# Performance work log

Hardware: AMD Instinct MI355X
Metric: run time of the kernel (lower is better)

## Reference

```python
import jax, jax.numpy as jnp
import numpy as np

WS = 8        # window size
NH = 8        # num heads


def setup_inputs() -> dict:
    key = jax.random.key(0)
    ks = jax.random.split(key, 6)
    B, C, H, W = 8, 256, 64, 64
    Cr = C // 4
    s = lambda n: 1.0 / np.sqrt(n)
    return {
        "x": jax.random.normal(ks[0], (B, C, H, W), jnp.float32),
        "ca_w1": jax.random.normal(ks[1], (Cr, C), jnp.float32) * s(C),
        "ca_b1": jnp.zeros((Cr,), jnp.float32),
        "ca_w2": jax.random.normal(ks[2], (C, Cr), jnp.float32) * s(Cr),
        "ca_b2": jnp.zeros((C,), jnp.float32),
        "in_proj_w": jax.random.normal(ks[3], (3 * C, C), jnp.float32) * s(C),
        "in_proj_b": jnp.zeros((3 * C,), jnp.float32),
        "out_proj_w": jax.random.normal(ks[4], (C, C), jnp.float32) * s(C),
        "out_proj_b": jnp.zeros((C,), jnp.float32),
    }


def reference(x, ca_w1, ca_b1, ca_w2, ca_b2, in_proj_w, in_proj_b, out_proj_w, out_proj_b):
    B, C, H, W = x.shape
    # ---- channel SE gate: AdaptiveAvgPool2d(1) -> 1x1 conv == linear ----
    pooled = x.mean(axis=(2, 3))                                   # [B, C]
    h1 = jax.nn.relu(pooled @ ca_w1.T + ca_b1)                     # [B, C/4]
    ca = jax.nn.sigmoid(h1 @ ca_w2.T + ca_b2)                      # [B, C]
    x = x * ca[:, :, None, None]

    # ---- window partition (non-overlapping unfold) ----
    Hw, Ww = H // WS, W // WS
    nwin = Hw * Ww
    xw = x.reshape(B, C, Hw, WS, Ww, WS).transpose(0, 1, 2, 4, 3, 5)   # [B,C,Hw,Ww,ws,ws]
    # view(B,C,nwin,ws*ws).permute(2,0,3,1).reshape(nwin*B, ws*ws, C)
    xw = xw.reshape(B, C, nwin, WS * WS).transpose(2, 0, 3, 1).reshape(nwin * B, WS * WS, C)

    # ---- nn.MultiheadAttention with batch_first=False: (L, N, E) ----
    # L = nwin*B (sequence!), N = ws*ws (batch!), E = C  -- faithful to source quirk
    L, N, _ = xw.shape
    hd = C // NH
    qkv = xw @ in_proj_w.T + in_proj_b                             # [L, N, 3C]
    q, k, v = jnp.split(qkv, 3, axis=-1)
    to_heads = lambda t: t.reshape(L, N, NH, hd).transpose(1, 2, 0, 3)  # [N, NH, L, hd]
    q, k, v = to_heads(q), to_heads(k), to_heads(v)
    scale = 1.0 / jnp.sqrt(jnp.asarray(hd, x.dtype))
    attn = jax.nn.softmax(jnp.einsum("nhld,nhmd->nhlm", q * scale, k), axis=-1)
    o = jnp.einsum("nhlm,nhmd->nhld", attn, v)                     # [N, NH, L, hd]
    o = o.transpose(2, 0, 1, 3).reshape(L, N, C)
    o = o @ out_proj_w.T + out_proj_b                              # [L, N, C]

    # ---- reshape back; nearest interpolate H*W -> H*W is identity ----
    o = o.reshape(nwin, B, WS * WS, C).transpose(1, 3, 0, 2)       # [B, C, nwin, ws*ws]
    x_out = o.reshape(B, C, H, W)
    return x + x_out
```

## Files before the change

kernel.cpp:

```cpp
#include <hip/hip_runtime.h>
#include <hip/hip_bf16.h>
#include <math.h>


typedef unsigned short ushort_t;
typedef unsigned int uint_t;
typedef __attribute__((ext_vector_type(8))) short bf16x8;
typedef __attribute__((ext_vector_type(4))) float f32x4;

__device__ __forceinline__ uint_t pk_trunc(float a, float b) {
    union { float f; uint_t u; } ua, ub; ua.f = a; ub.f = b;
    return (ua.u >> 16) | (ub.u & 0xffff0000u);
}

__device__ __forceinline__ uint_t pk_rne(float a, float b) {
    __hip_bfloat16 ha = __float2bfloat16(a), hb = __float2bfloat16(b);
    ushort_t ua = *(ushort_t*)&ha, ub = *(ushort_t*)&hb;
    return (uint_t)ua | ((uint_t)ub << 16);
}

__device__ __forceinline__ void gl_lds16(const ushort_t* g, ushort_t* l) {
    __builtin_amdgcn_global_load_lds(
        (__attribute__((address_space(1))) unsigned int*)(g),
        (__attribute__((address_space(3))) unsigned int*)(l), 16, 0, 0);
}

__global__ __launch_bounds__(256) void k_pool(const float* __restrict__ x,
                                              float* __restrict__ pooled) {
    int bc = blockIdx.x;
    const float4* row4 = (const float4*)(x + (size_t)bc * 4096);
    float s = 0.f;
    for (int i = threadIdx.x; i < 1024; i += 256) {
        float4 v = row4[i];
        s += v.x + v.y + v.z + v.w;
    }
    __shared__ float red[256];
    red[threadIdx.x] = s;
    __syncthreads();
    for (int o = 128; o > 0; o >>= 1) {
        if (threadIdx.x < o) red[threadIdx.x] += red[threadIdx.x + o];
        __syncthreads();
    }
    if (threadIdx.x == 0) pooled[bc] = red[0] * (1.f / 4096.f);
}

__global__ __launch_bounds__(256) void k_se(const float* __restrict__ pooled,
                                            const float* __restrict__ w1,
                                            const float* __restrict__ b1,
                                            const float* __restrict__ w2,
                                            const float* __restrict__ b2,
                                            float* __restrict__ ca) {
    __shared__ float sp[2048];
    __shared__ float sh1[512];
    int t = threadIdx.x;
    for (int i = t; i < 2048; i += 256) sp[i] = pooled[i];
    __syncthreads();
    for (int o = t; o < 512; o += 256) {
        int b = o >> 6, m = o & 63;
        float s = b1[m];
        const float* wr = w1 + (size_t)m * 256;
        const float* pr = sp + b * 256;
        for (int c = 0; c < 256; c++) s += pr[c] * wr[c];
        sh1[o] = s > 0.f ? s : 0.f;
    }
    __syncthreads();
    for (int o = t; o < 2048; o += 256) {
        int b = o >> 8, m = o & 255;
        float s = b2[m];
        const float* wr = w2 + (size_t)m * 64;
        const float* hr = sh1 + b * 64;
        for (int c = 0; c < 64; c++) s += hr[c] * wr[c];
        ca[o] = 1.f / (1.f + __expf(-s));
    }
}

__global__ __launch_bounds__(256) void k_cvt(const float* __restrict__ src,
                                             ushort_t* __restrict__ dst, int n8) {
    int i = blockIdx.x * 256 + threadIdx.x;
    if (i >= n8) return;
    const float4* s = (const float4*)src + (size_t)i * 2;
    float4 a = s[0], b = s[1];
    uint4 u;
    u.x = pk_rne(a.x, a.y); u.y = pk_rne(a.z, a.w);
    u.z = pk_rne(b.x, b.y); u.w = pk_rne(b.z, b.w);
    *(uint4*)(dst + (size_t)i * 8) = u;
}

#define GPAD 524
__global__ __launch_bounds__(256) void k_gate(const float* __restrict__ x,
                                              const float* __restrict__ ca,
                                              ushort_t* __restrict__ Ab) {
    __shared__ __align__(16) ushort_t Ls[32 * GPAD];
    __shared__ float sca[32];
    int bx = blockIdx.x;
    int b = bx >> 6, hw = (bx >> 3) & 7, c0 = (bx & 7) * 32;
    int t = threadIdx.x;
    if (t < 32) sca[t] = ca[b * 256 + c0 + t];
    __syncthreads();
    const float4* xb = (const float4*)(x + ((size_t)(b * 256 + c0) * 64 + hw * 8) * 64);
#pragma unroll
    for (int i = 0; i < 16; i++) {
        int f = i * 256 + t;
        int ch = f >> 7, rem = f & 127, r = rem >> 4, w4 = rem & 15;
        float4 v = xb[(size_t)ch * 1024 + r * 16 + w4];
        float g = sca[ch];
        uint2 u;
        u.x = pk_rne(v.x * g, v.y * g);
        u.y = pk_rne(v.z * g, v.w * g);
        *(uint2*)&Ls[ch * GPAD + r * 64 + w4 * 4] = u;
    }
    __syncthreads();
#pragma unroll
    for (int i = 0; i < 8; i++) {
        int q = i * 256 + t;
        int rr = q >> 2, part = q & 3;
        int ww = rr >> 6, p = rr & 63;
        int px = (p >> 3) * 64 + ww * 8 + (p & 7);
        const ushort_t* ls = &Ls[part * 8 * GPAD + px];
        uint4 u;
        u.x = (uint_t)ls[0]        | ((uint_t)ls[GPAD] << 16);
        u.y = (uint_t)ls[2 * GPAD] | ((uint_t)ls[3 * GPAD] << 16);
        u.z = (uint_t)ls[4 * GPAD] | ((uint_t)ls[5 * GPAD] << 16);
        u.w = (uint_t)ls[6 * GPAD] | ((uint_t)ls[7 * GPAD] << 16);
        size_t m = (size_t)(((hw * 8 + ww) * 8 + b) * 64 + p);
        *(uint4*)(Ab + m * 256 + c0 + part * 8) = u;
    }
}

__global__ __launch_bounds__(256, 2) void k_gemm_qkv2(const ushort_t* __restrict__ A,
                                                      const ushort_t* __restrict__ Bw,
                                                      const float* __restrict__ bias,
                                                      ushort_t* __restrict__ Qb,
                                                      ushort_t* __restrict__ Kb,
                                                      ushort_t* __restrict__ Vb) {
    __shared__ __align__(16) ushort_t As[128 * 64];
    __shared__ __align__(16) ushort_t Bs[128 * 64];
    int tid = threadIdx.x;
    int lane = tid & 63, wave = tid >> 6;
    int wm = wave >> 1, wn = wave & 1;
    int col = lane & 15, quad = lane >> 4;
    int n0 = blockIdx.x * 128;
    int m0 = blockIdx.y * 128;
    int cbase = wave * 64 + lane;

    f32x4 acc[4][4];
#pragma unroll
    for (int i = 0; i < 4; i++)
#pragma unroll
        for (int j = 0; j < 4; j++) acc[i][j] = (f32x4){0.f, 0.f, 0.f, 0.f};

    for (int k0 = 0; k0 < 256; k0 += 64) {
#pragma unroll
        for (int q = 0; q < 4; q++) {
            int c = q * 256 + cbase;
            int row = c >> 3;
            int kp = (c & 7) ^ (row & 7);
            gl_lds16(A + (size_t)(m0 + row) * 256 + k0 + kp * 8,
                     &As[(q * 4 + wave) * 512]);
            gl_lds16(Bw + (size_t)(n0 + row) * 256 + k0 + kp * 8,
                     &Bs[(q * 4 + wave) * 512]);
        }
        __syncthreads();
#pragma unroll
        for (int kk = 0; kk < 2; kk++) {
            bf16x8 af[4], bfg[4];
#pragma unroll
            for (int i = 0; i < 4; i++) {
                int row = wm * 64 + i * 16 + col;
                af[i] = *(const bf16x8*)&As[row * 64 + ((kk * 4 + quad) ^ (row & 7)) * 8];
            }
#pragma unroll
            for (int j = 0; j < 4; j++) {
                int row = wn * 64 + j * 16 + col;
                bfg[j] = *(const bf16x8*)&Bs[row * 64 + ((kk * 4 + quad) ^ (row & 7)) * 8];
            }
#pragma unroll
            for (int i = 0; i < 4; i++)
#pragma unroll
                for (int j = 0; j < 4; j++)
                    acc[i][j] = __builtin_amdgcn_mfma_f32_16x16x32_bf16(bfg[j], af[i], acc[i][j], 0, 0, 0);
        }
        __syncthreads();
    }

    int sec = n0 >> 8;
    ushort_t* dst = (sec == 0) ? Qb : (sec == 1) ? Kb : Vb;
    int nb = (n0 & 255) + wn * 64 + quad * 4;
#pragma unroll
    for (int j = 0; j < 4; j++) {
        float4 bv = *(const float4*)(bias + n0 + wn * 64 + j * 16 + quad * 4);
#pragma unroll
        for (int i = 0; i < 4; i++) {
            int m = m0 + wm * 64 + i * 16 + col;
            uint2 st;
            st.x = pk_rne(acc[i][j][0] + bv.x, acc[i][j][1] + bv.y);
            st.y = pk_rne(acc[i][j][2] + bv.z, acc[i][j][3] + bv.w);
            *(uint2*)(dst + (size_t)m * 256 + nb + j * 16) = st;
        }
    }
}

#define KS_STR 40
#define VT_STR 264
__global__ __launch_bounds__(256, 2) void k_attn(const ushort_t* __restrict__ Qb,
                                                 const ushort_t* __restrict__ Kb,
                                                 const ushort_t* __restrict__ Vb,
                                                 ushort_t* __restrict__ AO) {
    __shared__ __align__(16) ushort_t Ks[256 * KS_STR];
    __shared__ __align__(16) ushort_t Vt[32 * VT_STR];
    int p = blockIdx.x >> 3, h = blockIdx.x & 7;
    int tid = threadIdx.x;
    int lane = tid & 63, wave = tid >> 6;
    int col = lane & 15;
    int quad = lane >> 4;

    bf16x8 qfrag[8];
#pragma unroll
    for (int i = 0; i < 8; i++) {
        int qt = wave * 8 + i;
        qfrag[i] = *(const bf16x8*)(Qb + ((size_t)((qt * 16 + col) * 64 + p)) * 256 + h * 32 + quad * 8);
    }

    int R = col >> 2, r4 = lane & 3;
    int krow0 = 8 * R + r4;
    int krow1 = krow0 + 4;

    f32x4 O0[8], O1[8];
    float qsum[8];
#pragma unroll
    for (int i = 0; i < 8; i++) {
        O0[i] = (f32x4){0.f, 0.f, 0.f, 0.f};
        O1[i] = (f32x4){0.f, 0.f, 0.f, 0.f};
        qsum[i] = 0.f;
    }
    const float SC = 0.17677669529663687f;
    const f32x4 zero = {0.f, 0.f, 0.f, 0.f};

    for (int half = 0; half < 2; half++) {
        if (half) __syncthreads();
        for (int m = 0; m < 4; m++) {
            int T = m * 256 + tid;
            int key = T >> 2, oct = T & 3;
            size_t grow = ((size_t)((half * 256 + key) * 64 + p)) * 256 + h * 32 + oct * 8;
            *(bf16x8*)&Ks[key * KS_STR + oct * 8] = *(const bf16x8*)(Kb + grow);
            bf16x8 vv = *(const bf16x8*)(Vb + grow);
#pragma unroll
            for (int j = 0; j < 8; j++) Vt[(oct * 8 + j) * VT_STR + key] = (ushort_t)vv[j];
        }
        __syncthreads();

        for (int c = 0; c < 256; c += 32) {
            bf16x8 kf0 = *(const bf16x8*)&Ks[(c + krow0) * KS_STR + quad * 8];
            bf16x8 kf1 = *(const bf16x8*)&Ks[(c + krow1) * KS_STR + quad * 8];
            bf16x8 vf0 = *(const bf16x8*)&Vt[col * VT_STR + c + quad * 8];
            bf16x8 vf1 = *(const bf16x8*)&Vt[(col + 16) * VT_STR + c + quad * 8];
#pragma unroll
            for (int i = 0; i < 8; i++) {
                f32x4 s0 = __builtin_amdgcn_mfma_f32_16x16x32_bf16(kf0, qfrag[i], zero, 0, 0, 0);
                f32x4 s1 = __builtin_amdgcn_mfma_f32_16x16x32_bf16(kf1, qfrag[i], zero, 0, 0, 0);
                float p0[4], p1[4];
#pragma unroll
                for (int r = 0; r < 4; r++) {
                    p0[r] = __expf(s0[r] * SC);
                    p1[r] = __expf(s1[r] * SC);
                }
                qsum[i] += ((p0[0] + p0[1]) + (p0[2] + p0[3])) + ((p1[0] + p1[1]) + (p1[2] + p1[3]));
                union { uint_t u[4]; bf16x8 v; } pb;
                pb.u[0] = pk_trunc(p0[0], p0[1]);
                pb.u[1] = pk_trunc(p0[2], p0[3]);
                pb.u[2] = pk_trunc(p1[0], p1[1]);
                pb.u[3] = pk_trunc(p1[2], p1[3]);
                O0[i] = __builtin_amdgcn_mfma_f32_16x16x32_bf16(vf0, pb.v, O0[i], 0, 0, 0);
                O1[i] = __builtin_amdgcn_mfma_f32_16x16x32_bf16(vf1, pb.v, O1[i], 0, 0, 0);
            }
        }
    }

#pragma unroll
    for (int i = 0; i < 8; i++) {
        float s = qsum[i];
        s += __shfl_xor(s, 16);
        s += __shfl_xor(s, 32);
        float inv = 1.f / s;
        int qt = wave * 8 + i;
        ushort_t* dst = AO + ((size_t)((qt * 16 + col) * 64 + p)) * 256 + h * 32;
        uint2 st0, st1;
        st0.x = pk_rne(O0[i][0] * inv, O0[i][1] * inv);
        st0.y = pk_rne(O0[i][2] * inv, O0[i][3] * inv);
        st1.x = pk_rne(O1[i][0] * inv, O1[i][1] * inv);
        st1.y = pk_rne(O1[i][2] * inv, O1[i][3] * inv);
        *(uint2*)(dst + quad * 4) = st0;
        *(uint2*)(dst + 16 + quad * 4) = st1;
    }
}

__global__ __launch_bounds__(256, 2) void k_gemm_out2(const ushort_t* __restrict__ A,
                                                      const ushort_t* __restrict__ Bw,
                                                      const float* __restrict__ bias,
                                                      const float* __restrict__ x,
                                                      const float* __restrict__ ca,
                                                      float* __restrict__ out) {
    __shared__ __align__(16) ushort_t As[128 * 64];
    __shared__ __align__(16) ushort_t Bs[128 * 64];
    int tid = threadIdx.x;
    int lane = tid & 63, wave = tid >> 6;
    int wm = wave >> 1, wn = wave & 1;
    int col = lane & 15, quad = lane >> 4;
    int n0 = blockIdx.x * 128;
    int m0 = blockIdx.y * 128;
    int cbase = wave * 64 + lane;

    f32x4 acc[4][4];
#pragma unroll
    for (int i = 0; i < 4; i++)
#pragma unroll
        for (int j = 0; j < 4; j++) acc[i][j] = (f32x4){0.f, 0.f, 0.f, 0.f};

    for (int k0 = 0; k0 < 256; k0 += 64) {
#pragma unroll
        for (int q = 0; q < 4; q++) {
            int c = q * 256 + cbase;
            int row = c >> 3;
            int kp = (c & 7) ^ (row & 7);
            gl_lds16(A + (size_t)(m0 + row) * 256 + k0 + kp * 8,
                     &As[(q * 4 + wave) * 512]);
            gl_lds16(Bw + (size_t)(n0 + row) * 256 + k0 + kp * 8,
                     &Bs[(q * 4 + wave) * 512]);
        }
        __syncthreads();
#pragma unroll
        for (int kk = 0; kk < 2; kk++) {
            bf16x8 af[4], bfg[4];
#pragma unroll
            for (int i = 0; i < 4; i++) {
                int row = wm * 64 + i * 16 + col;
                af[i] = *(const bf16x8*)&As[row * 64 + ((kk * 4 + quad) ^ (row & 7)) * 8];
            }
#pragma unroll
            for (int j = 0; j < 4; j++) {
                int row = wn * 64 + j * 16 + col;
                bfg[j] = *(const bf16x8*)&Bs[row * 64 + ((kk * 4 + quad) ^ (row & 7)) * 8];
            }
#pragma unroll
            for (int i = 0; i < 4; i++)
#pragma unroll
                for (int j = 0; j < 4; j++)
                    acc[i][j] = __builtin_amdgcn_mfma_f32_16x16x32_bf16(bfg[j], af[i], acc[i][j], 0, 0, 0);
        }
        __syncthreads();
    }

    int lw = (m0 + wm * 64) >> 6;
    int b = lw & 7, w_idx = lw >> 3;
#pragma unroll
    for (int j = 0; j < 4; j++) {
        int nbase = n0 + wn * 64 + j * 16 + quad * 4;
        float4 bv = *(const float4*)(bias + nbase);
        float4 cv = *(const float4*)(ca + b * 256 + nbase);
#pragma unroll
        for (int i = 0; i < 4; i++) {
            int p = i * 16 + col;
#pragma unroll
            for (int r = 0; r < 4; r++) {
                int n = nbase + r;
                float bias_r = (r == 0) ? bv.x : (r == 1) ? bv.y : (r == 2) ? bv.z : bv.w;
                float ca_r = (r == 0) ? cv.x : (r == 1) ? cv.y : (r == 2) ? cv.z : cv.w;
                size_t oi = (((size_t)b * 256 + n) * 64 + w_idx) * 64 + p;
                out[oi] = acc[i][j][r] + bias_r + x[oi] * ca_r;
            }
        }
    }
}

extern "C" void kernel_launch(void* const* d_in, const int* in_sizes, int n_in,
                              void* d_out, int out_size, void* d_ws, size_t ws_size,
                              hipStream_t stream) {
    const float* x     = (const float*)d_in[0];
    const float* ca_w1 = (const float*)d_in[1];
    const float* ca_b1 = (const float*)d_in[2];
    const float* ca_w2 = (const float*)d_in[3];
    const float* ca_b2 = (const float*)d_in[4];
    const float* ipw   = (const float*)d_in[5];
    const float* ipb   = (const float*)d_in[6];
    const float* opw   = (const float*)d_in[7];
    const float* opb   = (const float*)d_in[8];
    float* out = (float*)d_out;

    char* ws = (char*)d_ws;
    const size_t MB16 = 16777216ull;
    ushort_t* Qb = (ushort_t*)(ws + 0);
    ushort_t* Kb = (ushort_t*)(ws + MB16);
    ushort_t* Vb = (ushort_t*)(ws + 2 * MB16);
    float* pooled = (float*)(ws + 3 * MB16);
    float* ca     = (float*)(ws + 3 * MB16 + 8192);

    ushort_t* Ab  = (ushort_t*)d_out;
    ushort_t* Wqb = (ushort_t*)((char*)d_out + MB16);
    ushort_t* Wob = Vb;

    k_cvt<<<96, 256, 0, stream>>>(ipw, Wqb, 24576);
    k_pool<<<2048, 256, 0, stream>>>(x, pooled);
    k_se<<<1, 256, 0, stream>>>(pooled, ca_w1, ca_b1, ca_w2, ca_b2, ca);
    k_gate<<<512, 256, 0, stream>>>(x, ca, Ab);
    k_gemm_qkv2<<<dim3(6, 256), 256, 0, stream>>>(Ab, Wqb, ipb, Qb, Kb, Vb);
    k_attn<<<512, 256, 0, stream>>>(Qb, Kb, Vb, Qb );
    k_cvt<<<32, 256, 0, stream>>>(opw, Wob, 8192);
    k_gemm_out2<<<dim3(2, 256), 256, 0, stream>>>(Qb, Wob, opb, x, ca, out);
}
```

Baseline: 215.2 us.

## Fold softmax scale into Q weights, widen attention block, swizzle LDS, use exp2

The softmax scale times log2(e) is folded into the Q part of the in-projection weights and bias during bf16 conversion, so the attention inner loop can call a raw exp2 instead of scale-multiply plus exp. The attention kernel now uses 512 threads and loads all 512 keys and values into LDS in one pass with XOR-swizzled layouts, which removes the two-half reload and its barrier. Each wave handles 4 query tiles instead of 8, cutting register use to allow more waves per CU. Probability packing uses a single perm instruction. This costs more LDS per block, and it changes rounding slightly because bf16 Q now carries the scale.

```diff
diff --git a/kernel.cpp b/kernel.cpp
--- a/kernel.cpp
+++ b/kernel.cpp
@@ -8,15 +8,17 @@
 typedef __attribute__((ext_vector_type(8))) short bf16x8;
 typedef __attribute__((ext_vector_type(4))) float f32x4;
 
-__device__ __forceinline__ uint_t pk_trunc(float a, float b) {
-    union { float f; uint_t u; } ua, ub; ua.f = a; ub.f = b;
-    return (ua.u >> 16) | (ub.u & 0xffff0000u);
-}
+#define ALPHA 0.25503486f
 
 __device__ __forceinline__ uint_t pk_rne(float a, float b) {
     __hip_bfloat16 ha = __float2bfloat16(a), hb = __float2bfloat16(b);
     ushort_t ua = *(ushort_t*)&ha, ub = *(ushort_t*)&hb;
     return (uint_t)ua | ((uint_t)ub << 16);
+}
+
+__device__ __forceinline__ uint_t pk2(float a, float b) {
+    union { float f; uint_t u; } ua, ub; ua.f = a; ub.f = b;
+    return __builtin_amdgcn_perm(ua.u, ub.u, 0x03020706u);
 }
 
 __device__ __forceinline__ void gl_lds16(const ushort_t* g, ushort_t* l) {
@@ -75,14 +77,16 @@
 }
 
 __global__ __launch_bounds__(256) void k_cvt(const float* __restrict__ src,
-                                             ushort_t* __restrict__ dst, int n8) {
+                                             ushort_t* __restrict__ dst, int n8,
+                                             int scale_n8, float scale) {
     int i = blockIdx.x * 256 + threadIdx.x;
     if (i >= n8) return;
+    float sc = (i < scale_n8) ? scale : 1.f;
     const float4* s = (const float4*)src + (size_t)i * 2;
     float4 a = s[0], b = s[1];
     uint4 u;
-    u.x = pk_rne(a.x, a.y); u.y = pk_rne(a.z, a.w);
-    u.z = pk_rne(b.x, b.y); u.w = pk_rne(b.z, b.w);
+    u.x = pk_rne(a.x * sc, a.y * sc); u.y = pk_rne(a.z * sc, a.w * sc);
+    u.z = pk_rne(b.x * sc, b.y * sc); u.w = pk_rne(b.z * sc, b.w * sc);
     *(uint4*)(dst + (size_t)i * 8) = u;
 }
 
@@ -185,10 +189,12 @@
 
     int sec = n0 >> 8;
     ushort_t* dst = (sec == 0) ? Qb : (sec == 1) ? Kb : Vb;
+    float bsc = (sec == 0) ? ALPHA : 1.f;
     int nb = (n0 & 255) + wn * 64 + quad * 4;
 #pragma unroll
     for (int j = 0; j < 4; j++) {
         float4 bv = *(const float4*)(bias + n0 + wn * 64 + j * 16 + quad * 4);
+        bv.x *= bsc; bv.y *= bsc; bv.z *= bsc; bv.w *= bsc;
 #pragma unroll
         for (int i = 0; i < 4; i++) {
             int m = m0 + wm * 64 + i * 16 + col;
@@ -200,89 +206,104 @@
     }
 }
 
-#define KS_STR 40
-#define VT_STR 264
-__global__ __launch_bounds__(256, 2) void k_attn(const ushort_t* __restrict__ Qb,
+__global__ __launch_bounds__(512, 4) void k_attn(const ushort_t* __restrict__ Qb,
                                                  const ushort_t* __restrict__ Kb,
                                                  const ushort_t* __restrict__ Vb,
                                                  ushort_t* __restrict__ AO) {
-    __shared__ __align__(16) ushort_t Ks[256 * KS_STR];
-    __shared__ __align__(16) ushort_t Vt[32 * VT_STR];
+    __shared__ __align__(16) ushort_t Ks[512 * 32];
+    __shared__ __align__(16) ushort_t Vt[32 * 512];
     int p = blockIdx.x >> 3, h = blockIdx.x & 7;
     int tid = threadIdx.x;
     int lane = tid & 63, wave = tid >> 6;
-    int col = lane & 15;
-    int quad = lane >> 4;
-
-    bf16x8 qfrag[8];
-#pragma unroll
-    for (int i = 0; i < 8; i++) {
-        int qt = wave * 8 + i;
+    int col = lane & 15, quad = lane >> 4;
+
+#pragma unroll
+    for (int it = 0; it < 4; it++) {
+        int u = it * 512 + tid;
+        int key = u >> 2, oct = u & 3;
+        size_t grow = ((size_t)(key * 64 + p)) * 256 + h * 32 + oct * 8;
+        int ck = oct ^ ((key >> 3) & 3);
+        *(bf16x8*)&Ks[key * 32 + ck * 8] = *(const bf16x8*)(Kb + grow);
+    }
+#pragma unroll
+    for (int it = 0; it < 2; it++) {
+        int u = it * 512 + tid;
+        int kp = u >> 2, oct = u & 3;
+        int k0 = kp * 2;
+        size_t g0 = ((size_t)(k0 * 64 + p)) * 256 + h * 32 + oct * 8;
+        bf16x8 v0 = *(const bf16x8*)(Vb + g0);
+        bf16x8 v1 = *(const bf16x8*)(Vb + g0 + 16384);
+        int kc = kp >> 2;
+#pragma unroll
+        for (int j = 0; j < 8; j++) {
+            int vc = oct * 8 + j;
+            int kcs = kc ^ (vc & 7) ^ ((vc >> 3) << 1);
+            uint_t pkv = (uint_t)(ushort_t)v0[j] | ((uint_t)(ushort_t)v1[j] << 16);
+            *(uint_t*)&Vt[vc * 512 + kcs * 8 + (k0 & 7)] = pkv;
+        }
+    }
+
+    bf16x8 qfrag[4];
+#pragma unroll
+    for (int i = 0; i < 4; i++) {
+        int qt = wave * 4 + i;
         qfrag[i] = *(const bf16x8*)(Qb + ((size_t)((qt * 16 + col) * 64 + p)) * 256 + h * 32 + quad * 8);
     }
 
-    int R = col >> 2, r4 = lane & 3;
-    int krow0 = 8 * R + r4;
-    int krow1 = krow0 + 4;
-
-    f32x4 O0[8], O1[8];
-    float qsum[8];
-#pragma unroll
-    for (int i = 0; i < 8; i++) {
+    f32x4 O0[4], O1[4];
+    float qsum[4];
+#pragma unroll
+    for (int i = 0; i < 4; i++) {
         O0[i] = (f32x4){0.f, 0.f, 0.f, 0.f};
         O1[i] = (f32x4){0.f, 0.f, 0.f, 0.f};
         qsum[i] = 0.f;
     }
-    const float SC = 0.17677669529663687f;
     const f32x4 zero = {0.f, 0.f, 0.f, 0.f};
-
-    for (int half = 0; half < 2; half++) {
-        if (half) __syncthreads();
-        for (int m = 0; m < 4; m++) {
-            int T = m * 256 + tid;
-            int key = T >> 2, oct = T & 3;
-            size_t grow = ((size_t)((half * 256 + key) * 64 + p)) * 256 + h * 32 + oct * 8;
-            *(bf16x8*)&Ks[key * KS_STR + oct * 8] = *(const bf16x8*)(Kb + grow);
-            bf16x8 vv = *(const bf16x8*)(Vb + grow);
-#pragma unroll
-            for (int j = 0; j < 8; j++) Vt[(oct * 8 + j) * VT_STR + key] = (ushort_t)vv[j];
-        }
-        __syncthreads();
-
-        for (int c = 0; c < 256; c += 32) {
-            bf16x8 kf0 = *(const bf16x8*)&Ks[(c + krow0) * KS_STR + quad * 8];
-            bf16x8 kf1 = *(const bf16x8*)&Ks[(c + krow1) * KS_STR + quad * 8];
-            bf16x8 vf0 = *(const bf16x8*)&Vt[col * VT_STR + c + quad * 8];
-            bf16x8 vf1 = *(const bf16x8*)&Vt[(col + 16) * VT_STR + c + quad * 8];
-#pragma unroll
-            for (int i = 0; i < 8; i++) {
-                f32x4 s0 = __builtin_amdgcn_mfma_f32_16x16x32_bf16(kf0, qfrag[i], zero, 0, 0, 0);
-                f32x4 s1 = __builtin_amdgcn_mfma_f32_16x16x32_bf16(kf1, qfrag[i], zero, 0, 0, 0);
-                float p0[4], p1[4];
-#pragma unroll
-                for (int r = 0; r < 4; r++) {
-                    p0[r] = __expf(s0[r] * SC);
-                    p1[r] = __expf(s1[r] * SC);
-                }
-                qsum[i] += ((p0[0] + p0[1]) + (p0[2] + p0[3])) + ((p1[0] + p1[1]) + (p1[2] + p1[3]));
-                union { uint_t u[4]; bf16x8 v; } pb;
-                pb.u[0] = pk_trunc(p0[0], p0[1]);
-                pb.u[1] = pk_trunc(p0[2], p0[3]);
-                pb.u[2] = pk_trunc(p1[0], p1[1]);
-                pb.u[3] = pk_trunc(p1[2], p1[3]);
-                O0[i] = __builtin_amdgcn_mfma_f32_16x16x32_bf16(vf0, pb.v, O0[i], 0, 0, 0);
-                O1[i] = __builtin_amdgcn_mfma_f32_16x16x32_bf16(vf1, pb.v, O1[i], 0, 0, 0);
-            }
-        }
-    }
-
-#pragma unroll
-    for (int i = 0; i < 8; i++) {
+    int R = col >> 2, r4 = lane & 3;
+    int krow0 = 8 * R + r4;
+    int vc0 = col, vc1 = col + 16;
+    int sw0 = (vc0 & 7) ^ ((vc0 >> 3) << 1);
+    int sw1 = (vc1 & 7) ^ ((vc1 >> 3) << 1);
+
+    __syncthreads();
+
+    for (int c = 0; c < 512; c += 32) {
+        int row0 = c + krow0;
+        int row1 = row0 + 4;
+        int ckq = quad ^ ((row0 >> 3) & 3);
+        bf16x8 kf0 = *(const bf16x8*)&Ks[row0 * 32 + ckq * 8];
+        bf16x8 kf1 = *(const bf16x8*)&Ks[row1 * 32 + ckq * 8];
+        int kc = (c >> 3) + quad;
+        bf16x8 vf0 = *(const bf16x8*)&Vt[vc0 * 512 + ((kc ^ sw0) * 8)];
+        bf16x8 vf1 = *(const bf16x8*)&Vt[vc1 * 512 + ((kc ^ sw1) * 8)];
+#pragma unroll
+        for (int i = 0; i < 4; i++) {
+            f32x4 s0 = __builtin_amdgcn_mfma_f32_16x16x32_bf16(kf0, qfrag[i], zero, 0, 0, 0);
+            f32x4 s1 = __builtin_amdgcn_mfma_f32_16x16x32_bf16(kf1, qfrag[i], zero, 0, 0, 0);
+            float p0[4], p1[4];
+#pragma unroll
+            for (int r = 0; r < 4; r++) {
+                p0[r] = __builtin_amdgcn_exp2f(s0[r]);
+                p1[r] = __builtin_amdgcn_exp2f(s1[r]);
+            }
+            qsum[i] += ((p0[0] + p0[1]) + (p0[2] + p0[3])) + ((p1[0] + p1[1]) + (p1[2] + p1[3]));
+            union { uint_t u[4]; bf16x8 v; } pb;
+            pb.u[0] = pk2(p0[0], p0[1]);
+            pb.u[1] = pk2(p0[2], p0[3]);
+            pb.u[2] = pk2(p1[0], p1[1]);
+            pb.u[3] = pk2(p1[2], p1[3]);
+            O0[i] = __builtin_amdgcn_mfma_f32_16x16x32_bf16(vf0, pb.v, O0[i], 0, 0, 0);
+            O1[i] = __builtin_amdgcn_mfma_f32_16x16x32_bf16(vf1, pb.v, O1[i], 0, 0, 0);
+        }
+    }
+
+#pragma unroll
+    for (int i = 0; i < 4; i++) {
         float s = qsum[i];
         s += __shfl_xor(s, 16);
         s += __shfl_xor(s, 32);
         float inv = 1.f / s;
-        int qt = wave * 8 + i;
+        int qt = wave * 4 + i;
         ushort_t* dst = AO + ((size_t)((qt * 16 + col) * 64 + p)) * 256 + h * 32;
         uint2 st0, st1;
         st0.x = pk_rne(O0[i][0] * inv, O0[i][1] * inv);
@@ -398,12 +419,12 @@
     ushort_t* Wqb = (ushort_t*)((char*)d_out + MB16);
     ushort_t* Wob = Vb;
 
-    k_cvt<<<96, 256, 0, stream>>>(ipw, Wqb, 24576);
+    k_cvt<<<96, 256, 0, stream>>>(ipw, Wqb, 24576, 8192, ALPHA);
     k_pool<<<2048, 256, 0, stream>>>(x, pooled);
     k_se<<<1, 256, 0, stream>>>(pooled, ca_w1, ca_b1, ca_w2, ca_b2, ca);
     k_gate<<<512, 256, 0, stream>>>(x, ca, Ab);
     k_gemm_qkv2<<<dim3(6, 256), 256, 0, stream>>>(Ab, Wqb, ipb, Qb, Kb, Vb);
-    k_attn<<<512, 256, 0, stream>>>(Qb, Kb, Vb, Qb );
-    k_cvt<<<32, 256, 0, stream>>>(opw, Wob, 8192);
+    k_attn<<<512, 512, 0, stream>>>(Qb, Kb, Vb, Qb );
+    k_cvt<<<32, 256, 0, stream>>>(opw, Wob, 8192, 0, 1.f);
     k_gemm_out2<<<dim3(2, 256), 256, 0, stream>>>(Qb, Wob, opb, x, ca, out);
 }
```

Result: faster. 206.8 us (-3.9%).
